# Performance work log

Measured on AMD Instinct MI355X. Metric: run time of the kernel, lower is better.

The kernel has to match this reference:

```python
import jax, jax.numpy as jnp
import numpy as np

D_LUT = 33  # 3D LUT resolution per axis


def setup_inputs() -> dict:
    key = jax.random.key(0)
    k1, k2 = jax.random.split(key)
    lut = jax.random.normal(k1, (3, D_LUT, D_LUT, D_LUT), dtype=jnp.float32)
    img = jax.random.uniform(k2, (32, 3, 512, 512), dtype=jnp.float32)
    return {"lut": lut, "img": img}


def _trilerp(lut, img):
    # Faithful port of F.grid_sample(lut_5d, grid, mode='bilinear',
    # padding_mode='border', align_corners=True) with grid = img*2-1 permuted.
    # grid last-dim order is (x, y, z): r indexes the LAST lut axis, g the
    # second-to-last, b the depth axis. lut: [3, D, D, D], img: [B, 3, H, W].
    D = lut.shape[1]
    s = jnp.float32(D - 1)
    # align_corners=True: unnormalized coord = (grid+1)/2*(D-1) = channel*(D-1)
    # border padding: clamp coordinates to the valid range.
    r, g, b = img[:, 0], img[:, 1], img[:, 2]           # each [B, H, W]
    x = jnp.clip(r * s, 0.0, s)
    y = jnp.clip(g * s, 0.0, s)
    z = jnp.clip(b * s, 0.0, s)

    x0 = jnp.clip(jnp.floor(x), 0.0, s - 1.0)
    y0 = jnp.clip(jnp.floor(y), 0.0, s - 1.0)
    z0 = jnp.clip(jnp.floor(z), 0.0, s - 1.0)
    wx = x - x0
    wy = y - y0
    wz = z - z0

    x0i = x0.astype(jnp.int32); x1i = x0i + 1
    y0i = y0.astype(jnp.int32); y1i = y0i + 1
    z0i = z0.astype(jnp.int32); z1i = z0i + 1

    def corner(zi, yi, xi):
        return lut[:, zi, yi, xi]  # [3, B, H, W] gather

    # trilinear blend of 8 corners; weights [B,H,W] broadcast over channel dim
    out = (corner(z0i, y0i, x0i) * (1 - wz) * (1 - wy) * (1 - wx)
           + corner(z0i, y0i, x1i) * (1 - wz) * (1 - wy) * wx
           + corner(z0i, y1i, x0i) * (1 - wz) * wy * (1 - wx)
           + corner(z0i, y1i, x1i) * (1 - wz) * wy * wx
           + corner(z1i, y0i, x0i) * wz * (1 - wy) * (1 - wx)
           + corner(z1i, y0i, x1i) * wz * (1 - wy) * wx
           + corner(z1i, y1i, x0i) * wz * wy * (1 - wx)
           + corner(z1i, y1i, x1i) * wz * wy * wx)
    return jnp.transpose(out, (1, 0, 2, 3))  # [B, 3, H, W]


def reference(lut, img):
    out = _trilerp(lut, img)
    return (lut, out)
```

## Files before the change

### kernel.cpp

```cpp
#include <hip/hip_runtime.h>
#include <hip/hip_fp16.h>


constexpr int D = 33;
constexpr int LUT_C_STRIDE = D * D * D;
constexpr int LUT_N = 3 * LUT_C_STRIDE;
constexpr int HW = 512 * 512;
constexpr int NPIX = 32 * HW;
constexpr int NCELL = 32 * 32 * 32;
constexpr size_t TABLE_BYTES = (size_t)NCELL * 64;

__global__ __launch_bounds__(256)
void build_cells_kernel(const float* __restrict__ lut, __half* __restrict__ tbl) {
    int cell = blockIdx.x * 256 + threadIdx.x;
    if (cell >= NCELL) return;
    int x0 = cell & 31;
    int y0 = (cell >> 5) & 31;
    int z0 = cell >> 10;
    int base = z0 * (D * D) + y0 * D + x0;
    __half* dst = tbl + (size_t)cell * 32;
#pragma unroll
    for (int c = 0; c < 3; ++c) {
        const float* L = lut + c * LUT_C_STRIDE + base;
        dst[c * 8 + 0] = __float2half(L[0]);
        dst[c * 8 + 1] = __float2half(L[1]);
        dst[c * 8 + 2] = __float2half(L[D]);
        dst[c * 8 + 3] = __float2half(L[D + 1]);
        dst[c * 8 + 4] = __float2half(L[D * D]);
        dst[c * 8 + 5] = __float2half(L[D * D + 1]);
        dst[c * 8 + 6] = __float2half(L[D * D + D]);
        dst[c * 8 + 7] = __float2half(L[D * D + D + 1]);
    }
}

__device__ __forceinline__ float lerp3(const float* v, float wx, float wy, float wz) {
    float c00 = v[0] + wx * (v[1] - v[0]);
    float c01 = v[2] + wx * (v[3] - v[2]);
    float c10 = v[4] + wx * (v[5] - v[4]);
    float c11 = v[6] + wx * (v[7] - v[6]);
    float c0 = c00 + wy * (c01 - c00);
    float c1 = c10 + wy * (c11 - c10);
    return c0 + wz * (c1 - c0);
}

__global__ __launch_bounds__(256)
void trilerp_cells_kernel(const uint4* __restrict__ tbl,
                          const float* __restrict__ img,
                          float* __restrict__ out) {
    int p = blockIdx.x * 256 + threadIdx.x;
    if (p >= NPIX) return;
    int b = p >> 18;
    int hw = p & (HW - 1);
    const float* ip = img + (size_t)b * (3 * HW) + hw;
    float r = ip[0];
    float g = ip[HW];
    float bl = ip[2 * HW];

    const float s = 32.0f;
    float x = fminf(fmaxf(r * s, 0.0f), s);
    float y = fminf(fmaxf(g * s, 0.0f), s);
    float z = fminf(fmaxf(bl * s, 0.0f), s);
    float xf = fminf(floorf(x), 31.0f);
    float yf = fminf(floorf(y), 31.0f);
    float zf = fminf(floorf(z), 31.0f);
    float wx = x - xf, wy = y - yf, wz = z - zf;
    int ix = (int)xf, iy = (int)yf, iz = (int)zf;
    int cell = (iz << 10) | (iy << 5) | ix;

    const uint4* cp = tbl + (size_t)cell * 4;
    union {
        uint4 q[3];
        __half h[24];
    } u;
    u.q[0] = cp[0];
    u.q[1] = cp[1];
    u.q[2] = cp[2];

    float v[8];
    float res[3];
#pragma unroll
    for (int c = 0; c < 3; ++c) {
#pragma unroll
        for (int i = 0; i < 8; ++i) v[i] = __half2float(u.h[c * 8 + i]);
        res[c] = lerp3(v, wx, wy, wz);
    }

    float* op = out + (size_t)b * (3 * HW) + hw;
    op[0] = res[0];
    op[HW] = res[1];
    op[2 * HW] = res[2];
}

__global__ __launch_bounds__(256)
void trilerp_direct_kernel(const float* __restrict__ lut,
                           const float* __restrict__ img,
                           float* __restrict__ out) {
    int p = blockIdx.x * 256 + threadIdx.x;
    if (p >= NPIX) return;
    int b = p >> 18;
    int hw = p & (HW - 1);
    const float* ip = img + (size_t)b * (3 * HW) + hw;
    float r = ip[0];
    float g = ip[HW];
    float bl = ip[2 * HW];

    const float s = 32.0f;
    float x = fminf(fmaxf(r * s, 0.0f), s);
    float y = fminf(fmaxf(g * s, 0.0f), s);
    float z = fminf(fmaxf(bl * s, 0.0f), s);
    float xf = fminf(floorf(x), 31.0f);
    float yf = fminf(floorf(y), 31.0f);
    float zf = fminf(floorf(z), 31.0f);
    float wx = x - xf, wy = y - yf, wz = z - zf;
    int ix = (int)xf, iy = (int)yf, iz = (int)zf;
    int base = iz * (D * D) + iy * D + ix;

    float* op = out + (size_t)b * (3 * HW) + hw;
#pragma unroll
    for (int c = 0; c < 3; ++c) {
        const float* L = lut + c * LUT_C_STRIDE + base;
        float v[8];
        v[0] = L[0];
        v[1] = L[1];
        v[2] = L[D];
        v[3] = L[D + 1];
        v[4] = L[D * D];
        v[5] = L[D * D + 1];
        v[6] = L[D * D + D];
        v[7] = L[D * D + D + 1];
        op[c * HW] = lerp3(v, wx, wy, wz);
    }
}

extern "C" void kernel_launch(void* const* d_in, const int* in_sizes, int n_in,
                              void* d_out, int out_size, void* d_ws, size_t ws_size,
                              hipStream_t stream) {
    const float* lut = (const float*)d_in[0];
    const float* img = (const float*)d_in[1];
    float* out = (float*)d_out;

    hipMemcpyAsync(d_out, d_in[0], (size_t)LUT_N * sizeof(float),
                   hipMemcpyDeviceToDevice, stream);

    float* out_img = out + LUT_N;

    if (ws_size >= TABLE_BYTES) {
        build_cells_kernel<<<(NCELL + 255) / 256, 256, 0, stream>>>(
            lut, (__half*)d_ws);
        trilerp_cells_kernel<<<(NPIX + 255) / 256, 256, 0, stream>>>(
            (const uint4*)d_ws, img, out_img);
    } else {
        trilerp_direct_kernel<<<(NPIX + 255) / 256, 256, 0, stream>>>(
            lut, img, out_img);
    }
}
```

Baseline: 219.1 us.

## Vectorize trilerp to 4 pixels per thread and fold LUT copy into build kernel

Each thread in the cell-table trilerp kernel now handles four consecutive pixels. It uses 128-bit nontemporal loads for the image channels and 128-bit nontemporal stores for the output, and issues the twelve table gathers together to expose memory-level parallelism. The separate device-to-device memcpy of the LUT into the output is removed and done inside the table-build kernel, which saves one launch/copy operation. The cost is more registers per thread and a quarter as many threads. The grid also assumes NPIX divides evenly by 4*256, so the bounds check is gone.

New measurement: 233.6 us. +6.6%, slower.

```diff
diff --git a/kernel.cpp b/kernel.cpp
--- a/kernel.cpp
+++ b/kernel.cpp
@@ -10,15 +10,19 @@
 constexpr int NCELL = 32 * 32 * 32;
 constexpr size_t TABLE_BYTES = (size_t)NCELL * 64;
 
+typedef float f32x4 __attribute__((ext_vector_type(4)));
+
 __global__ __launch_bounds__(256)
-void build_cells_kernel(const float* __restrict__ lut, __half* __restrict__ tbl) {
-    int cell = blockIdx.x * 256 + threadIdx.x;
-    if (cell >= NCELL) return;
-    int x0 = cell & 31;
-    int y0 = (cell >> 5) & 31;
-    int z0 = cell >> 10;
+void build_cells_kernel(const float* __restrict__ lut, __half* __restrict__ tbl,
+                        float* __restrict__ lut_out) {
+    int tid = blockIdx.x * 256 + threadIdx.x;
+    if (tid < LUT_N) lut_out[tid] = lut[tid];
+    if (tid >= NCELL) return;
+    int x0 = tid & 31;
+    int y0 = (tid >> 5) & 31;
+    int z0 = tid >> 10;
     int base = z0 * (D * D) + y0 * D + x0;
-    __half* dst = tbl + (size_t)cell * 32;
+    __half* dst = tbl + (size_t)tid * 32;
 #pragma unroll
     for (int c = 0; c < 3; ++c) {
         const float* L = lut + c * LUT_C_STRIDE + base;
@@ -47,48 +51,60 @@
 void trilerp_cells_kernel(const uint4* __restrict__ tbl,
                           const float* __restrict__ img,
                           float* __restrict__ out) {
-    int p = blockIdx.x * 256 + threadIdx.x;
-    if (p >= NPIX) return;
-    int b = p >> 18;
-    int hw = p & (HW - 1);
+    int t = blockIdx.x * 256 + threadIdx.x;
+    int b = t >> 16;
+    int hw = (t & 65535) << 2;
     const float* ip = img + (size_t)b * (3 * HW) + hw;
-    float r = ip[0];
-    float g = ip[HW];
-    float bl = ip[2 * HW];
+
+    f32x4 r  = __builtin_nontemporal_load((const f32x4*)(ip));
+    f32x4 g  = __builtin_nontemporal_load((const f32x4*)(ip + HW));
+    f32x4 bl = __builtin_nontemporal_load((const f32x4*)(ip + 2 * HW));
 
     const float s = 32.0f;
-    float x = fminf(fmaxf(r * s, 0.0f), s);
-    float y = fminf(fmaxf(g * s, 0.0f), s);
-    float z = fminf(fmaxf(bl * s, 0.0f), s);
-    float xf = fminf(floorf(x), 31.0f);
-    float yf = fminf(floorf(y), 31.0f);
-    float zf = fminf(floorf(z), 31.0f);
-    float wx = x - xf, wy = y - yf, wz = z - zf;
-    int ix = (int)xf, iy = (int)yf, iz = (int)zf;
-    int cell = (iz << 10) | (iy << 5) | ix;
+    int cell[4];
+    float wx[4], wy[4], wz[4];
+#pragma unroll
+    for (int i = 0; i < 4; ++i) {
+        float x = fminf(fmaxf(r[i] * s, 0.0f), s);
+        float y = fminf(fmaxf(g[i] * s, 0.0f), s);
+        float z = fminf(fmaxf(bl[i] * s, 0.0f), s);
+        float xf = fminf(floorf(x), 31.0f);
+        float yf = fminf(floorf(y), 31.0f);
+        float zf = fminf(floorf(z), 31.0f);
+        wx[i] = x - xf; wy[i] = y - yf; wz[i] = z - zf;
+        cell[i] = (((int)zf) << 10) | (((int)yf) << 5) | ((int)xf);
+    }
 
-    const uint4* cp = tbl + (size_t)cell * 4;
-    union {
-        uint4 q[3];
-        __half h[24];
-    } u;
-    u.q[0] = cp[0];
-    u.q[1] = cp[1];
-    u.q[2] = cp[2];
+    uint4 q0[4], q1[4], q2[4];
+#pragma unroll
+    for (int i = 0; i < 4; ++i) {
+        const uint4* cp = tbl + (size_t)cell[i] * 4;
+        q0[i] = cp[0];
+        q1[i] = cp[1];
+        q2[i] = cp[2];
+    }
 
-    float v[8];
-    float res[3];
+    f32x4 res0, res1, res2;
 #pragma unroll
-    for (int c = 0; c < 3; ++c) {
+    for (int i = 0; i < 4; ++i) {
+        union { uint4 q[3]; __half h[24]; } u;
+        u.q[0] = q0[i]; u.q[1] = q1[i]; u.q[2] = q2[i];
+        float v[8];
 #pragma unroll
-        for (int i = 0; i < 8; ++i) v[i] = __half2float(u.h[c * 8 + i]);
-        res[c] = lerp3(v, wx, wy, wz);
+        for (int k = 0; k < 8; ++k) v[k] = __half2float(u.h[k]);
+        res0[i] = lerp3(v, wx[i], wy[i], wz[i]);
+#pragma unroll
+        for (int k = 0; k < 8; ++k) v[k] = __half2float(u.h[8 + k]);
+        res1[i] = lerp3(v, wx[i], wy[i], wz[i]);
+#pragma unroll
+        for (int k = 0; k < 8; ++k) v[k] = __half2float(u.h[16 + k]);
+        res2[i] = lerp3(v, wx[i], wy[i], wz[i]);
     }
 
     float* op = out + (size_t)b * (3 * HW) + hw;
-    op[0] = res[0];
-    op[HW] = res[1];
-    op[2 * HW] = res[2];
+    __builtin_nontemporal_store(res0, (f32x4*)(op));
+    __builtin_nontemporal_store(res1, (f32x4*)(op + HW));
+    __builtin_nontemporal_store(res2, (f32x4*)(op + 2 * HW));
 }
 
 __global__ __launch_bounds__(256)
@@ -112,22 +128,17 @@
     float yf = fminf(floorf(y), 31.0f);
     float zf = fminf(floorf(z), 31.0f);
     float wx = x - xf, wy = y - yf, wz = z - zf;
-    int ix = (int)xf, iy = (int)yf, iz = (int)zf;
-    int base = iz * (D * D) + iy * D + ix;
+    int base = ((int)zf) * (D * D) + ((int)yf) * D + (int)xf;
 
     float* op = out + (size_t)b * (3 * HW) + hw;
 #pragma unroll
     for (int c = 0; c < 3; ++c) {
         const float* L = lut + c * LUT_C_STRIDE + base;
         float v[8];
-        v[0] = L[0];
-        v[1] = L[1];
-        v[2] = L[D];
-        v[3] = L[D + 1];
-        v[4] = L[D * D];
-        v[5] = L[D * D + 1];
-        v[6] = L[D * D + D];
-        v[7] = L[D * D + D + 1];
+        v[0] = L[0];        v[1] = L[1];
+        v[2] = L[D];        v[3] = L[D + 1];
+        v[4] = L[D * D];    v[5] = L[D * D + 1];
+        v[6] = L[D * D + D]; v[7] = L[D * D + D + 1];
         op[c * HW] = lerp3(v, wx, wy, wz);
     }
 }
@@ -138,18 +149,16 @@
     const float* lut = (const float*)d_in[0];
     const float* img = (const float*)d_in[1];
     float* out = (float*)d_out;
-
-    hipMemcpyAsync(d_out, d_in[0], (size_t)LUT_N * sizeof(float),
-                   hipMemcpyDeviceToDevice, stream);
-
     float* out_img = out + LUT_N;
 
     if (ws_size >= TABLE_BYTES) {
-        build_cells_kernel<<<(NCELL + 255) / 256, 256, 0, stream>>>(
-            lut, (__half*)d_ws);
-        trilerp_cells_kernel<<<(NPIX + 255) / 256, 256, 0, stream>>>(
+        build_cells_kernel<<<(LUT_N + 255) / 256, 256, 0, stream>>>(
+            lut, (__half*)d_ws, out);
+        trilerp_cells_kernel<<<NPIX / 4 / 256, 256, 0, stream>>>(
             (const uint4*)d_ws, img, out_img);
     } else {
+        hipMemcpyAsync(d_out, d_in[0], (size_t)LUT_N * sizeof(float),
+                       hipMemcpyDeviceToDevice, stream);
         trilerp_direct_kernel<<<(NPIX + 255) / 256, 256, 0, stream>>>(
             lut, img, out_img);
     }
```
